# Kernel tuning notes

Hardware: AMD Instinct MI355X
Metric: run time of the kernel (lower is better)

Reference implementation:

```python
import jax, jax.numpy as jnp
import numpy as np

N_PF, N_GW, N_SW = 60000, 300000, 60000
D_IN, D, E = 32, 64, 1_000_000


def _mk_edge(key, n_src, n_dst, n_edges):
    k1, k2 = jax.random.split(key)
    return jnp.stack([
        jax.random.randint(k1, (n_edges,), 0, n_src),
        jax.random.randint(k2, (n_edges,), 0, n_dst),
    ]).astype(jnp.int32)


def _self_edge(n):
    r = jnp.arange(n, dtype=jnp.int32)
    return jnp.stack([r, r])


def setup_inputs() -> dict:
    key = jax.random.key(0)
    ks = jax.random.split(key, 20)
    s = 0.05
    return {
        "x_pf": jax.random.normal(ks[0], (N_PF, D_IN), jnp.float32),
        "x_gw": jax.random.normal(ks[1], (N_GW, D_IN), jnp.float32),
        "x_sw": jax.random.normal(ks[2], (N_SW, D_IN), jnp.float32),
        "W1l": jax.random.normal(ks[3], (10, D, D_IN), jnp.float32) * s,
        "b1l": jax.random.normal(ks[4], (10, D), jnp.float32) * s,
        "W1r": jax.random.normal(ks[5], (10, D, D_IN), jnp.float32) * s,
        "W2l": jax.random.normal(ks[6], (10, D, D), jnp.float32) * s,
        "b2l": jax.random.normal(ks[7], (10, D), jnp.float32) * s,
        "W2r": jax.random.normal(ks[8], (10, D, D), jnp.float32) * s,
        "lin_W": jax.random.normal(ks[9], (1, D), jnp.float32) * s,
        "lin_b": jax.random.normal(ks[10], (1,), jnp.float32) * s,
        "prelu_a": jnp.float32(0.25),
        "ei_pf_gw": _mk_edge(ks[11], N_PF, N_GW, E),
        "ei_gw_pf": _mk_edge(ks[12], N_GW, N_PF, E),
        "ei_pf_sw": _mk_edge(ks[13], N_PF, N_SW, E),
        "ei_sw_pf": _mk_edge(ks[14], N_SW, N_PF, E),
        "ei_sw_gw": _mk_edge(ks[15], N_SW, N_GW, E),
        "ei_gw_sw": _mk_edge(ks[16], N_GW, N_SW, E),
        "ei_gw_gw": _mk_edge(ks[17], N_GW, N_GW, E),
        "ei_gw_self": _self_edge(N_GW),
        "ei_sw_self": _self_edge(N_SW),
        "ei_pf_self": _self_edge(N_PF),
    }


def reference(x_pf, x_gw, x_sw, W1l, b1l, W1r, W2l, b2l, W2r, lin_W, lin_b,
              prelu_a, ei_pf_gw, ei_gw_pf, ei_pf_sw, ei_sw_pf, ei_sw_gw,
              ei_gw_sw, ei_gw_gw, ei_gw_self, ei_sw_self, ei_pf_self):
    n_pf, n_gw, n_sw = x_pf.shape[0], x_gw.shape[0], x_sw.shape[0]

    def sage(x_src, x_dst, ei, Wl, bl, Wr, n_dst):
        # PyG SAGEConv: lin_l(mean_j x_j) + lin_r(x_i); lin_r has no bias
        msg = x_src[ei[0]]                                        # [E, Din]
        summed = jax.ops.segment_sum(msg, ei[1], num_segments=n_dst)
        cnt = jax.ops.segment_sum(jnp.ones(ei.shape[1], x_src.dtype), ei[1],
                                  num_segments=n_dst)
        mean = summed / jnp.maximum(cnt, 1.0)[:, None]            # [Ndst, Din]
        return mean @ Wl.T + bl + x_dst @ Wr.T

    def layer(h_pf, h_gw, h_sw, Wl, bl, Wr):
        # HeteroConv with aggr='sum' over edge types per destination node type
        out_gw = (sage(h_pf, h_gw, ei_pf_gw, Wl[0], bl[0], Wr[0], n_gw)
                  + sage(h_sw, h_gw, ei_sw_gw, Wl[4], bl[4], Wr[4], n_gw)
                  + sage(h_gw, h_gw, ei_gw_gw, Wl[6], bl[6], Wr[6], n_gw)
                  + sage(h_gw, h_gw, ei_gw_self, Wl[7], bl[7], Wr[7], n_gw))
        out_pf = (sage(h_gw, h_pf, ei_gw_pf, Wl[1], bl[1], Wr[1], n_pf)
                  + sage(h_sw, h_pf, ei_sw_pf, Wl[3], bl[3], Wr[3], n_pf)
                  + sage(h_pf, h_pf, ei_pf_self, Wl[9], bl[9], Wr[9], n_pf))
        out_sw = (sage(h_pf, h_sw, ei_pf_sw, Wl[2], bl[2], Wr[2], n_sw)
                  + sage(h_gw, h_sw, ei_gw_sw, Wl[5], bl[5], Wr[5], n_sw)
                  + sage(h_sw, h_sw, ei_sw_self, Wl[8], bl[8], Wr[8], n_sw))
        return out_pf, out_gw, out_sw

    h_pf, h_gw, h_sw = layer(x_pf, x_gw, x_sw, W1l, b1l, W1r)
    h_pf, h_gw, h_sw = jax.nn.relu(h_pf), jax.nn.relu(h_gw), jax.nn.relu(h_sw)
    h_pf, h_gw, h_sw = layer(h_pf, h_gw, h_sw, W2l, b2l, W2r)
    h_pf, h_gw, h_sw = jax.nn.relu(h_pf), jax.nn.relu(h_gw), jax.nn.relu(h_sw)

    def prelu(v):
        return jnp.where(v >= 0, v, prelu_a * v)

    out_gw = prelu(h_gw @ lin_W.T + lin_b)   # [N_GW, 1]
    out_sw = prelu(h_sw @ lin_W.T + lin_b)   # [N_SW, 1]
    return out_gw, out_sw, h_pf
```

## Files before the change

kernel.cpp:

```cpp
#include <hip/hip_runtime.h>

typedef __attribute__((ext_vector_type(8))) short short8;
typedef __attribute__((ext_vector_type(4))) float floatx4;

#define N_PF 60000
#define N_GW 300000
#define N_SW 60000
#define EPT 1000000
#define TOTE 7000000
#define L_CNT 1140000
#define SPAN 4096
#define N_B 279
#define CHSZ 4096
#define NCH 1709

__device__ __forceinline__ unsigned short f2bf(float f) {
  unsigned u = __float_as_uint(f);
  u = (u + 0x7FFF + ((u >> 16) & 1)) >> 16;
  return (unsigned short)u;
}
__device__ __forceinline__ float bf2f(unsigned short u) {
  return __uint_as_float((unsigned)u << 16);
}
__device__ __forceinline__ void acc8(float* a, short8 v) {
#pragma unroll
  for (int k = 0; k < 8; ++k) a[k] += bf2f((unsigned short)v[k]);
}

__device__ __forceinline__ int cnt_base(int et) {
  switch (et) {
    case 0: return 0;
    case 1: return 300000;
    case 2: return 360000;
    case 3: return 420000;
    case 4: return 480000;
    case 5: return 780000;
    default: return 840000;
  }
}

__device__ __forceinline__ const int* pick(const int* e0, const int* e1,
                                           const int* e2, const int* e3,
                                           const int* e4, const int* e5,
                                           const int* e6, int et) {
  switch (et) {
    case 0: return e0; case 1: return e1; case 2: return e2; case 3: return e3;
    case 4: return e4; case 5: return e5; default: return e6;
  }
}

__global__ __launch_bounds__(256) void k_cast(const float4* __restrict__ x,
                                              ushort4* __restrict__ xb, int n4) {
  int i = blockIdx.x * 256 + threadIdx.x;
  if (i < n4) {
    float4 v = x[i];
    ushort4 o;
    o.x = f2bf(v.x); o.y = f2bf(v.y); o.z = f2bf(v.z); o.w = f2bf(v.w);
    xb[i] = o;
  }
}


__global__ __launch_bounds__(256) void k_h1(
    const int* e0, const int* e1, const int* e2, const int* e3,
    const int* e4, const int* e5, const int* e6, int* __restrict__ hcnt) {
  __shared__ int hist[N_B];
  int ch = blockIdx.x, t = threadIdx.x;
  for (int i = t; i < N_B; i += 256) hist[i] = 0;
  __syncthreads();
  int base = ch * CHSZ;
  int nn = TOTE - base; if (nn > CHSZ) nn = CHSZ;
#pragma unroll
  for (int u = 0; u < CHSZ / 256; ++u) {
    int o = u * 256 + t;
    if (o < nn) {
      int gid = base + o;
      int et = gid / EPT, i2 = gid - et * EPT;
      const int* ei = pick(e0, e1, e2, e3, e4, e5, e6, et);
      int idx = cnt_base(et) + ei[EPT + i2];
      atomicAdd(&hist[idx >> 12], 1);
    }
  }
  __syncthreads();
  for (int b = t; b < N_B; b += 256) hcnt[(size_t)b * NCH + ch] = hist[b];
}

__global__ __launch_bounds__(256) void k_h2a(const int* __restrict__ hcnt,
                                             int* __restrict__ btot) {
  __shared__ int sh[4];
  int b = blockIdx.x;
  const int* c = hcnt + (size_t)b * NCH;
  int s = 0;
  for (int k = threadIdx.x; k < NCH; k += 256) s += c[k];
  for (int off = 1; off < 64; off <<= 1) s += __shfl_xor(s, off, 64);
  int lane = threadIdx.x & 63, w = threadIdx.x >> 6;
  if (lane == 0) sh[w] = s;
  __syncthreads();
  if (threadIdx.x == 0) btot[b] = sh[0] + sh[1] + sh[2] + sh[3];
}

__global__ __launch_bounds__(64) void k_h2b(const int* __restrict__ btot,
                                            int* __restrict__ bbase,
                                            int* __restrict__ Sarr) {
  int lane = threadIdx.x;
  int v[5]; int s = 0;
#pragma unroll
  for (int k = 0; k < 5; ++k) {
    int i = lane * 5 + k;
    v[k] = (i < N_B) ? btot[i] : 0;
    s += v[k];
  }
  int x = s;
  for (int off = 1; off < 64; off <<= 1) {
    int tv = __shfl_up(x, off, 64);
    if (lane >= off) x += tv;
  }
  int run = x - s;
#pragma unroll
  for (int k = 0; k < 5; ++k) {
    int i = lane * 5 + k;
    if (i < N_B) bbase[i] = run;
    run += v[k];
  }
  if (lane == 63) { bbase[N_B] = x; Sarr[L_CNT] = TOTE; }
}

__global__ __launch_bounds__(256) void k_h2c(int* __restrict__ hcnt,
                                             const int* __restrict__ bbase) {
  __shared__ int sc[256];
  int b = blockIdx.x, t = threadIdx.x;
  int* c = hcnt + (size_t)b * NCH;
  int v[7]; int s = 0;
#pragma unroll
  for (int k = 0; k < 7; ++k) {
    int i = t * 7 + k;
    v[k] = (i < NCH) ? c[i] : 0;
    s += v[k];
  }
  sc[t] = s;
  __syncthreads();
  for (int off = 1; off < 256; off <<= 1) {
    int tv = (t >= off) ? sc[t - off] : 0;
    __syncthreads();
    sc[t] += tv;
    __syncthreads();
  }
  int run = bbase[b] + sc[t] - s;
#pragma unroll
  for (int k = 0; k < 7; ++k) {
    int i = t * 7 + k;
    if (i < NCH) { int vv = v[k]; c[i] = run; run += vv; }
  }
}

__global__ __launch_bounds__(256) void k_bfill(
    const int* e0, const int* e1, const int* e2, const int* e3,
    const int* e4, const int* e5, const int* e6,
    const int* __restrict__ hcnt, unsigned* __restrict__ part) {
  __shared__ int hist[N_B];
  __shared__ int segs[N_B];
  __shared__ int curb[N_B];
  __shared__ int gbase[N_B];
  __shared__ int sc[256];
  __shared__ unsigned long long stg[CHSZ];
  int ch = blockIdx.x, t = threadIdx.x;
  for (int i = t; i < N_B; i += 256) hist[i] = 0;
  __syncthreads();
  int base = ch * CHSZ;
  int nn = TOTE - base; if (nn > CHSZ) nn = CHSZ;
#pragma unroll
  for (int u = 0; u < CHSZ / 256; ++u) {
    int o = u * 256 + t;
    if (o < nn) {
      int gid = base + o;
      int et = gid / EPT, i2 = gid - et * EPT;
      const int* ei = pick(e0, e1, e2, e3, e4, e5, e6, et);
      int idx = cnt_base(et) + ei[EPT + i2];
      atomicAdd(&hist[idx >> 12], 1);
    }
  }
  __syncthreads();
  int v0 = (2 * t < N_B) ? hist[2 * t] : 0;
  int v1 = (2 * t + 1 < N_B) ? hist[2 * t + 1] : 0;
  int s = v0 + v1;
  sc[t] = s;
  __syncthreads();
  for (int off = 1; off < 256; off <<= 1) {
    int tv = (t >= off) ? sc[t - off] : 0;
    __syncthreads();
    sc[t] += tv;
    __syncthreads();
  }
  int excl = sc[t] - s;
  if (2 * t < N_B) { segs[2 * t] = excl; curb[2 * t] = excl; }
  if (2 * t + 1 < N_B) { segs[2 * t + 1] = excl + v0; curb[2 * t + 1] = excl + v0; }
  for (int b = t; b < N_B; b += 256) gbase[b] = hcnt[(size_t)b * NCH + ch];
  __syncthreads();
#pragma unroll
  for (int u = 0; u < CHSZ / 256; ++u) {
    int o = u * 256 + t;
    if (o < nn) {
      int gid = base + o;
      int et = gid / EPT, i2 = gid - et * EPT;
      const int* ei = pick(e0, e1, e2, e3, e4, e5, e6, et);
      int dst = ei[EPT + i2];
      int src = ei[i2];
      int idx = cnt_base(et) + dst;
      unsigned long long p = ((unsigned long long)idx << 32) | (unsigned)src;
      int r = atomicAdd(&curb[idx >> 12], 1);
      stg[r] = p;
    }
  }
  __syncthreads();
  for (int sdx = t; sdx < nn; sdx += 256) {
    unsigned long long p = stg[sdx];
    int idx = (int)(p >> 32);
    int b = idx >> 12;
    unsigned ent = ((unsigned)(idx & 4095) << 19) | (unsigned)(p & 0x7FFFF);
    part[(size_t)gbase[b] + (sdx - segs[b])] = ent;
  }
}

__global__ __launch_bounds__(1024) void k_cfill(
    const unsigned* __restrict__ part, const int* __restrict__ bbase,
    int* __restrict__ Sarr, int* __restrict__ col) {
  __shared__ int hist[SPAN];
  __shared__ int wt[16];
  int t = threadIdx.x;
  int lane = t & 63, wv = t >> 6;
  int b = blockIdx.x;
  int lo = b * SPAN;
  int span_n = L_CNT - lo; if (span_n > SPAN) span_n = SPAN;
  int s0 = bbase[b], s1 = bbase[b + 1];
  ((int4*)hist)[t] = (int4){0, 0, 0, 0};
  __syncthreads();
  for (int j = s0 + t; j < s1; j += 1024) {
    int local = (int)(part[j] >> 19);
    atomicAdd(&hist[local], 1);
  }
  __syncthreads();
  int4 v = ((int4*)hist)[t];
  int s = v.x + v.y + v.z + v.w;
  int x = s;
#pragma unroll
  for (int off = 1; off < 64; off <<= 1) {
    int tv = __shfl_up(x, off, 64);
    if (lane >= off) x += tv;
  }
  if (lane == 63) wt[wv] = x;
  __syncthreads();
  int woff = 0;
#pragma unroll
  for (int k = 0; k < 16; ++k) woff += (k < wv) ? wt[k] : 0;
  int run = woff + x - s;
  int4 cur4, sa4;
  cur4.x = run; sa4.x = s0 + run; run += v.x;
  cur4.y = run; sa4.y = s0 + run; run += v.y;
  cur4.z = run; sa4.z = s0 + run; run += v.z;
  cur4.w = run; sa4.w = s0 + run; run += v.w;
  __syncthreads();
  ((int4*)hist)[t] = cur4;
  if (t * 4 + 3 < span_n) {
    *(int4*)(&Sarr[lo + t * 4]) = sa4;
  } else {
    if (t * 4 + 0 < span_n) Sarr[lo + t * 4 + 0] = sa4.x;
    if (t * 4 + 1 < span_n) Sarr[lo + t * 4 + 1] = sa4.y;
    if (t * 4 + 2 < span_n) Sarr[lo + t * 4 + 2] = sa4.z;
  }
  __syncthreads();
  for (int j = s0 + t; j < s1; j += 1024) {
    unsigned p = part[j];
    int local = (int)(p >> 19);
    int r = atomicAdd(&hist[local], 1);
    col[s0 + r] = (int)(p & 0x7FFFF);
  }
}

template <int KIN, int NE>
__global__ __launch_bounds__(256) void k_prep(
    const float* __restrict__ Wl, const float* __restrict__ Wr,
    const float* __restrict__ bl, int e0, int e1, int e2, int es,
    unsigned short* __restrict__ wsw, float* __restrict__ bias) {
  constexpr int KCAT = (NE + 1) * KIN;
  int idx = blockIdx.x * 256 + threadIdx.x;
  if (idx < KCAT * 64) {
    int j = idx & 7, lane = (idx >> 3) & 63, t = idx >> 9;
    int ct = t & 3, kc = t >> 2;
    int k = kc * 32 + ((lane >> 4) << 3) + j;
    int c = ct * 16 + (lane & 15);
    int seg = k / KIN, kk = k - seg * KIN;
    float v;
    if (seg < NE) {
      int e = (seg == 0) ? e0 : (seg == 1) ? e1 : e2;
      v = Wl[((size_t)e * 64 + c) * KIN + kk];
    } else {
      v = Wl[((size_t)es * 64 + c) * KIN + kk] +
          Wr[((size_t)es * 64 + c) * KIN + kk] +
          Wr[((size_t)e0 * 64 + c) * KIN + kk] +
          Wr[((size_t)e1 * 64 + c) * KIN + kk];
      if (NE == 3) v += Wr[((size_t)e2 * 64 + c) * KIN + kk];
    }
    wsw[idx] = f2bf(v);
  } else if (idx < KCAT * 64 + 64) {
    int c = idx - KCAT * 64;
    float v = bl[e0 * 64 + c] + bl[e1 * 64 + c] + bl[es * 64 + c];
    if (NE == 3) v += bl[e2 * 64 + c];
    bias[c] = v;
  }
}

struct LType {
  const unsigned short* s0;
  const unsigned short* s1;
  const unsigned short* s2;
  int b0, b1, b2, ne;
  const unsigned short* xD;
  const unsigned short* wsw;
  const float* bias;
  void* hOut;
  int omode;
  int ntile;
};

template <int KIN, int MINW>
__global__ __launch_bounds__(256, MINW) void k_layerF(
    const int* __restrict__ Sarr, const int* __restrict__ col, LType t0,
    LType t1, LType t2, const float* __restrict__ linW,
    const float* __restrict__ linb, const float* __restrict__ pa) {
  constexpr int ZSTR = KIN + 8;
  constexpr int LPR = KIN / 8;
  constexpr int G = 64 / LPR;
  constexpr int KD = KIN / 32;
  __shared__ unsigned short z[4 * 16 * ZSTR];
  const int lane = threadIdx.x & 63;
  unsigned short* zw = &z[(threadIdx.x >> 6) * 16 * ZSTR];
  const int wid = (blockIdx.x * 256 + threadIdx.x) >> 6;
  const int nw = (gridDim.x * 256) >> 6;
  const int cl = lane & 15, quad = lane >> 4;
  const int g = lane / LPR;
  const int c = lane % LPR;
  const int TT = t0.ntile + t1.ntile + t2.ntile;

  for (int tile = wid; tile < TT; tile += nw) {
    LType tp;
    int lt = tile;
    if (lt < t0.ntile) tp = t0;
    else if ((lt -= t0.ntile) < t1.ntile) tp = t1;
    else { lt -= t1.ntile; tp = t2; }
    const int nb = lt * 16;
    const int ne = tp.ne;
    const int klds = ne * KD;

    floatx4 acc[4];
#pragma unroll
    for (int ct = 0; ct < 4; ++ct) {
      float bv = tp.bias[ct * 16 + cl];
      acc[ct] = (floatx4){bv, bv, bv, bv};
    }
#pragma unroll
    for (int kd = 0; kd < KD; ++kd) {
      short8 a = *(const short8*)(tp.xD + (size_t)(nb + cl) * KIN +
                                  kd * 32 + quad * 8);
      int kc = klds + kd;
#pragma unroll
      for (int ct = 0; ct < 4; ++ct) {
        short8 b =
            *(const short8*)(tp.wsw + ((size_t)(kc * 4 + ct) * 64 + lane) * 8);
        acc[ct] = __builtin_amdgcn_mfma_f32_16x16x32_bf16(a, b, acc[ct], 0, 0, 0);
      }
    }

#pragma unroll
    for (int E = 0; E < 3; ++E) {
      if (E < ne) {
        const unsigned short* se = (E == 0) ? tp.s0 : (E == 1) ? tp.s1 : tp.s2;
        int be = (E == 0) ? tp.b0 : (E == 1) ? tp.b1 : tp.b2;
#pragma unroll
        for (int i0 = 0; i0 < 16; i0 += G) {
          int n = nb + i0 + g;
          unsigned short* zr = &zw[(i0 + g) * ZSTR];
          int s = Sarr[be + n];
          int t = Sarr[be + n + 1];
          float a0[8] = {0, 0, 0, 0, 0, 0, 0, 0};
          float a1[8] = {0, 0, 0, 0, 0, 0, 0, 0};
          int j = s;
          for (; j + 1 < t; j += 2) {
            int r0 = col[j], r1 = col[j + 1];
            short8 v0 = *(const short8*)(se + (size_t)r0 * KIN + c * 8);
            short8 v1 = *(const short8*)(se + (size_t)r1 * KIN + c * 8);
            acc8(a0, v0);
            acc8(a1, v1);
          }
          if (j < t) {
            int r0 = col[j];
            short8 v0 = *(const short8*)(se + (size_t)r0 * KIN + c * 8);
            acc8(a0, v0);
          }
          int cv = t - s;
          if (cv < 1) cv = 1;
          float inv = 1.0f / (float)cv;
          short8 o;
#pragma unroll
          for (int k = 0; k < 8; ++k)
            o[k] = (short)f2bf((a0[k] + a1[k]) * inv);
          *(short8*)(&zr[c * 8]) = o;
        }
#pragma unroll
        for (int kc2 = 0; kc2 < KD; ++kc2) {
          short8 a = *(const short8*)(&zw[cl * ZSTR + kc2 * 32 + quad * 8]);
          int kc = E * KD + kc2;
#pragma unroll
          for (int ct = 0; ct < 4; ++ct) {
            short8 b = *(const short8*)(tp.wsw +
                                        ((size_t)(kc * 4 + ct) * 64 + lane) * 8);
            acc[ct] =
                __builtin_amdgcn_mfma_f32_16x16x32_bf16(a, b, acc[ct], 0, 0, 0);
          }
        }
      }
    }
    if (tp.omode == 2) {
      float p[4] = {0.f, 0.f, 0.f, 0.f};
#pragma unroll
      for (int ct = 0; ct < 4; ++ct) {
        float w = linW[ct * 16 + cl];
#pragma unroll
        for (int r = 0; r < 4; ++r) {
          float v = acc[ct][r];
          v = v > 0.f ? v : 0.f;
          p[r] += v * w;
        }
      }
#pragma unroll
      for (int off = 1; off < 16; off <<= 1) {
#pragma unroll
        for (int r = 0; r < 4; ++r) p[r] += __shfl_xor(p[r], off, 64);
      }
      if (cl == 0) {
        float lb = linb[0], al = pa[0];
        float* o = (float*)tp.hOut;
#pragma unroll
        for (int r = 0; r < 4; ++r) {
          int n = nb + quad * 4 + r;
          float v = p[r] + lb;
          o[n] = v >= 0.f ? v : al * v;
        }
      }
    } else if (tp.omode == 1) {
#pragma unroll
      for (int ct = 0; ct < 4; ++ct)
#pragma unroll
        for (int r = 0; r < 4; ++r) {
          int n = nb + quad * 4 + r;
          float v = acc[ct][r];
          ((float*)tp.hOut)[(size_t)n * 64 + ct * 16 + cl] = v > 0.f ? v : 0.f;
        }
    } else {
#pragma unroll
      for (int ct = 0; ct < 4; ++ct)
#pragma unroll
        for (int r = 0; r < 4; ++r) {
          int n = nb + quad * 4 + r;
          float v = acc[ct][r];
          ((unsigned short*)tp.hOut)[(size_t)n * 64 + ct * 16 + cl] =
              f2bf(v > 0.f ? v : 0.f);
        }
    }
  }
}

extern "C" void kernel_launch(void* const* d_in, const int* in_sizes, int n_in,
                              void* d_out, int out_size, void* d_ws,
                              size_t ws_size, hipStream_t stream) {
  const float* x_pf = (const float*)d_in[0];
  const float* x_gw = (const float*)d_in[1];
  const float* x_sw = (const float*)d_in[2];
  const float* W1l = (const float*)d_in[3];
  const float* b1l = (const float*)d_in[4];
  const float* W1r = (const float*)d_in[5];
  const float* W2l = (const float*)d_in[6];
  const float* b2l = (const float*)d_in[7];
  const float* W2r = (const float*)d_in[8];
  const float* linW = (const float*)d_in[9];
  const float* linb = (const float*)d_in[10];
  const float* pa = (const float*)d_in[11];
  const int* e0 = (const int*)d_in[12];
  const int* e1 = (const int*)d_in[13];
  const int* e2 = (const int*)d_in[14];
  const int* e3 = (const int*)d_in[15];
  const int* e4 = (const int*)d_in[16];
  const int* e5 = (const int*)d_in[17];
  const int* e6 = (const int*)d_in[18];
  float* out = (float*)d_out;

  char* w = (char*)d_ws;
  size_t off = 0;
  auto alloc = [&](size_t bytes) -> void* {
    void* p = w + off;
    off += bytes;
    off = (off + 255) & ~(size_t)255;
    return p;
  };
  unsigned* part = (unsigned*)alloc((size_t)TOTE * 4);
  int* col = (int*)alloc((size_t)TOTE * 4);
  int* Sarr = (int*)alloc((size_t)(L_CNT + 1) * 4);
  int* hcnt = (int*)alloc((size_t)N_B * NCH * 4);
  int* btot = (int*)alloc((N_B + 1) * 4);
  int* bbase = (int*)alloc((N_B + 1) * 4);
  unsigned short* xb_pf = (unsigned short*)alloc((size_t)N_PF * 32 * 2);
  unsigned short* xb_gw = (unsigned short*)alloc((size_t)N_GW * 32 * 2);
  unsigned short* xb_sw = (unsigned short*)alloc((size_t)N_SW * 32 * 2);
  unsigned short* h1_pf = (unsigned short*)alloc((size_t)N_PF * 64 * 2);
  unsigned short* h1_gw = (unsigned short*)alloc((size_t)N_GW * 64 * 2);
  unsigned short* h1_sw = (unsigned short*)alloc((size_t)N_SW * 64 * 2);
  unsigned short* w1gw = (unsigned short*)alloc(128 * 64 * 2);
  unsigned short* w1pf = (unsigned short*)alloc(96 * 64 * 2);
  unsigned short* w1sw = (unsigned short*)alloc(96 * 64 * 2);
  unsigned short* w2gw = (unsigned short*)alloc(256 * 64 * 2);
  unsigned short* w2pf = (unsigned short*)alloc(192 * 64 * 2);
  unsigned short* w2sw = (unsigned short*)alloc(192 * 64 * 2);
  float* bs1gw = (float*)alloc(64 * 4);
  float* bs1pf = (float*)alloc(64 * 4);
  float* bs1sw = (float*)alloc(64 * 4);
  float* bs2gw = (float*)alloc(64 * 4);
  float* bs2pf = (float*)alloc(64 * 4);
  float* bs2sw = (float*)alloc(64 * 4);

  k_cast<<<(N_PF * 8 + 255) / 256, 256, 0, stream>>>((const float4*)x_pf,
                                                     (ushort4*)xb_pf, N_PF * 8);
  k_cast<<<(N_GW * 8 + 255) / 256, 256, 0, stream>>>((const float4*)x_gw,
                                                     (ushort4*)xb_gw, N_GW * 8);
  k_cast<<<(N_SW * 8 + 255) / 256, 256, 0, stream>>>((const float4*)x_sw,
                                                     (ushort4*)xb_sw, N_SW * 8);

  k_h1<<<NCH, 256, 0, stream>>>(e0, e1, e2, e3, e4, e5, e6, hcnt);
  k_h2a<<<N_B, 256, 0, stream>>>(hcnt, btot);
  k_h2b<<<1, 64, 0, stream>>>(btot, bbase, Sarr);
  k_h2c<<<N_B, 256, 0, stream>>>(hcnt, bbase);
  k_bfill<<<NCH, 256, 0, stream>>>(e0, e1, e2, e3, e4, e5, e6, hcnt, part);
  k_cfill<<<N_B, 1024, 0, stream>>>(part, bbase, Sarr, col);

  k_prep<32, 3><<<(128 * 64 + 64 + 255) / 256, 256, 0, stream>>>(
      W1l, W1r, b1l, 0, 4, 6, 7, w1gw, bs1gw);
  k_prep<32, 2><<<(96 * 64 + 64 + 255) / 256, 256, 0, stream>>>(
      W1l, W1r, b1l, 1, 3, 0, 9, w1pf, bs1pf);
  k_prep<32, 2><<<(96 * 64 + 64 + 255) / 256, 256, 0, stream>>>(
      W1l, W1r, b1l, 2, 5, 0, 8, w1sw, bs1sw);
  k_prep<64, 3><<<(256 * 64 + 64 + 255) / 256, 256, 0, stream>>>(
      W2l, W2r, b2l, 0, 4, 6, 7, w2gw, bs2gw);
  k_prep<64, 2><<<(192 * 64 + 64 + 255) / 256, 256, 0, stream>>>(
      W2l, W2r, b2l, 1, 3, 0, 9, w2pf, bs2pf);
  k_prep<64, 2><<<(192 * 64 + 64 + 255) / 256, 256, 0, stream>>>(
      W2l, W2r, b2l, 2, 5, 0, 8, w2sw, bs2sw);

  LType a0{xb_pf, xb_sw, xb_gw, 0, 480000, 840000, 3,
           xb_gw, w1gw, bs1gw, h1_gw, 0, N_GW / 16};
  LType a1{xb_gw, xb_sw, nullptr, 300000, 420000, 0, 2,
           xb_pf, w1pf, bs1pf, h1_pf, 0, N_PF / 16};
  LType a2{xb_pf, xb_gw, nullptr, 360000, 780000, 0, 2,
           xb_sw, w1sw, bs1sw, h1_sw, 0, N_SW / 16};
  k_layerF<32, 8><<<2048, 256, 0, stream>>>(Sarr, col, a0, a1, a2, linW, linb,
                                            pa);

  LType c0{h1_pf, h1_sw, h1_gw, 0, 480000, 840000, 3,
           h1_gw, w2gw, bs2gw, out, 2, N_GW / 16};
  LType c1{h1_gw, h1_sw, nullptr, 300000, 420000, 0, 2,
           h1_pf, w2pf, bs2pf, out + 360000, 1, N_PF / 16};
  LType c2{h1_pf, h1_gw, nullptr, 360000, 780000, 0, 2,
           h1_sw, w2sw, bs2sw, out + N_GW, 2, N_SW / 16};
  k_layerF<64, 8><<<2048, 256, 0, stream>>>(Sarr, col, c0, c1, c2, linW, linb,
                                            pa);
}
```

Baseline: 721.8 us.

## Gather neighbor means directly into MFMA A-fragments, removing LDS staging

Each lane now aggregates neighbors for its own MFMA row (cl) and k-slice (quad), so the mean-aggregated features land directly in register A-fragments instead of being written to shared memory and re-read. All CSR offsets for the row are loaded up front, and the root-feature MFMA is moved after the neighbor MFMAs. This removes LDS traffic and the shared buffer, but changes the gather pattern: 4 lanes now work per row instead of spreading a row across LPR lanes. That gives less memory-level parallelism per row and possibly more per-lane degree imbalance, and register pressure rises.

```diff
diff --git a/kernel.cpp b/kernel.cpp
--- a/kernel.cpp
+++ b/kernel.cpp
@@ -327,18 +327,11 @@
     const int* __restrict__ Sarr, const int* __restrict__ col, LType t0,
     LType t1, LType t2, const float* __restrict__ linW,
     const float* __restrict__ linb, const float* __restrict__ pa) {
-  constexpr int ZSTR = KIN + 8;
-  constexpr int LPR = KIN / 8;
-  constexpr int G = 64 / LPR;
   constexpr int KD = KIN / 32;
-  __shared__ unsigned short z[4 * 16 * ZSTR];
   const int lane = threadIdx.x & 63;
-  unsigned short* zw = &z[(threadIdx.x >> 6) * 16 * ZSTR];
   const int wid = (blockIdx.x * 256 + threadIdx.x) >> 6;
   const int nw = (gridDim.x * 256) >> 6;
   const int cl = lane & 15, quad = lane >> 4;
-  const int g = lane / LPR;
-  const int c = lane % LPR;
   const int TT = t0.ntile + t1.ntile + t2.ntile;
 
   for (int tile = wid; tile < TT; tile += nw) {
@@ -350,50 +343,56 @@
     const int nb = lt * 16;
     const int ne = tp.ne;
     const int klds = ne * KD;
-
-    floatx4 acc[4];
-#pragma unroll
-    for (int ct = 0; ct < 4; ++ct) {
-      float bv = tp.bias[ct * 16 + cl];
-      acc[ct] = (floatx4){bv, bv, bv, bv};
-    }
-#pragma unroll
-    for (int kd = 0; kd < KD; ++kd) {
-      short8 a = *(const short8*)(tp.xD + (size_t)(nb + cl) * KIN +
-                                  kd * 32 + quad * 8);
-      int kc = klds + kd;
-#pragma unroll
-      for (int ct = 0; ct < 4; ++ct) {
-        short8 b =
-            *(const short8*)(tp.wsw + ((size_t)(kc * 4 + ct) * 64 + lane) * 8);
-        acc[ct] = __builtin_amdgcn_mfma_f32_16x16x32_bf16(a, b, acc[ct], 0, 0, 0);
-      }
-    }
-
+    const int nrow = nb + cl;
+
+    int sE[3], tE[3];
+    sE[0] = Sarr[tp.b0 + nrow]; tE[0] = Sarr[tp.b0 + nrow + 1];
+    sE[1] = Sarr[tp.b1 + nrow]; tE[1] = Sarr[tp.b1 + nrow + 1];
+    sE[2] = 0; tE[2] = 0;
+    if (ne == 3) { sE[2] = Sarr[tp.b2 + nrow]; tE[2] = Sarr[tp.b2 + nrow + 1]; }
+
+    short8 fr[3][KD];
 #pragma unroll
     for (int E = 0; E < 3; ++E) {
       if (E < ne) {
         const unsigned short* se = (E == 0) ? tp.s0 : (E == 1) ? tp.s1 : tp.s2;
-        int be = (E == 0) ? tp.b0 : (E == 1) ? tp.b1 : tp.b2;
-#pragma unroll
-        for (int i0 = 0; i0 < 16; i0 += G) {
-          int n = nb + i0 + g;
-          unsigned short* zr = &zw[(i0 + g) * ZSTR];
-          int s = Sarr[be + n];
-          int t = Sarr[be + n + 1];
+        const int s = sE[E], t = tE[E];
+        if (KD == 2) {
+          float a0[8] = {0, 0, 0, 0, 0, 0, 0, 0};
+          float a1[8] = {0, 0, 0, 0, 0, 0, 0, 0};
+          for (int j = s; j < t; ++j) {
+            int r = col[j];
+            const unsigned short* p = se + (size_t)r * KIN + quad * 8;
+            short8 v0 = *(const short8*)(p);
+            short8 v1 = *(const short8*)(p + 32);
+            acc8(a0, v0);
+            acc8(a1, v1);
+          }
+          int cv = t - s;
+          if (cv < 1) cv = 1;
+          float inv = 1.0f / (float)cv;
+          short8 o0, o1;
+#pragma unroll
+          for (int k = 0; k < 8; ++k) {
+            o0[k] = (short)f2bf(a0[k] * inv);
+            o1[k] = (short)f2bf(a1[k] * inv);
+          }
+          fr[E][0] = o0;
+          fr[E][KD - 1] = o1;
+        } else {
           float a0[8] = {0, 0, 0, 0, 0, 0, 0, 0};
           float a1[8] = {0, 0, 0, 0, 0, 0, 0, 0};
           int j = s;
           for (; j + 1 < t; j += 2) {
             int r0 = col[j], r1 = col[j + 1];
-            short8 v0 = *(const short8*)(se + (size_t)r0 * KIN + c * 8);
-            short8 v1 = *(const short8*)(se + (size_t)r1 * KIN + c * 8);
+            short8 v0 = *(const short8*)(se + (size_t)r0 * KIN + quad * 8);
+            short8 v1 = *(const short8*)(se + (size_t)r1 * KIN + quad * 8);
             acc8(a0, v0);
             acc8(a1, v1);
           }
           if (j < t) {
             int r0 = col[j];
-            short8 v0 = *(const short8*)(se + (size_t)r0 * KIN + c * 8);
+            short8 v0 = *(const short8*)(se + (size_t)r0 * KIN + quad * 8);
             acc8(a0, v0);
           }
           int cv = t - s;
@@ -401,14 +400,25 @@
           float inv = 1.0f / (float)cv;
           short8 o;
 #pragma unroll
-          for (int k = 0; k < 8; ++k)
-            o[k] = (short)f2bf((a0[k] + a1[k]) * inv);
-          *(short8*)(&zr[c * 8]) = o;
+          for (int k = 0; k < 8; ++k) o[k] = (short)f2bf((a0[k] + a1[k]) * inv);
+          fr[E][0] = o;
         }
-#pragma unroll
-        for (int kc2 = 0; kc2 < KD; ++kc2) {
-          short8 a = *(const short8*)(&zw[cl * ZSTR + kc2 * 32 + quad * 8]);
-          int kc = E * KD + kc2;
+      }
+    }
+
+    floatx4 acc[4];
+#pragma unroll
+    for (int ct = 0; ct < 4; ++ct) {
+      float bv = tp.bias[ct * 16 + cl];
+      acc[ct] = (floatx4){bv, bv, bv, bv};
+    }
+#pragma unroll
+    for (int E = 0; E < 3; ++E) {
+      if (E < ne) {
+#pragma unroll
+        for (int kd = 0; kd < KD; ++kd) {
+          short8 a = fr[E][kd];
+          int kc = E * KD + kd;
 #pragma unroll
           for (int ct = 0; ct < 4; ++ct) {
             short8 b = *(const short8*)(tp.wsw +
@@ -417,6 +427,18 @@
                 __builtin_amdgcn_mfma_f32_16x16x32_bf16(a, b, acc[ct], 0, 0, 0);
           }
         }
+      }
+    }
+#pragma unroll
+    for (int kd = 0; kd < KD; ++kd) {
+      short8 a = *(const short8*)(tp.xD + (size_t)nrow * KIN + kd * 32 +
+                                  quad * 8);
+      int kc = klds + kd;
+#pragma unroll
+      for (int ct = 0; ct < 4; ++ct) {
+        short8 b =
+            *(const short8*)(tp.wsw + ((size_t)(kc * 4 + ct) * 64 + lane) * 8);
+        acc[ct] = __builtin_amdgcn_mfma_f32_16x16x32_bf16(a, b, acc[ct], 0, 0, 0);
       }
     }
     if (tp.omode == 2) {
```

Result: no change. 733.0 us (+1.5%).
